# Kernel tuning notes

Hardware: AMD Instinct MI355X
Metric: run time of the kernel (lower is better)

The kernel has to match this reference:

```python
import jax, jax.numpy as jnp
import numpy as np

N = 1024
H = 128


def setup_inputs() -> dict:
    key = jax.random.key(0)
    k1, k2, k3, k4, k5, k6 = jax.random.split(key, 6)
    s = 1.0 / np.sqrt(H)
    return {
        "node_feats": jax.random.normal(k1, (N, H), dtype=jnp.float32),
        "edge_attr": jax.random.normal(k2, (N * N, H), dtype=jnp.float32),
        "We": jax.random.uniform(k3, (H, H), jnp.float32, -s, s),
        "be": jax.random.uniform(k4, (H,), jnp.float32, -s, s),
        "Wi": jax.random.uniform(k5, (H, H), jnp.float32, -s, s),
        "Wj": jax.random.uniform(k6, (H, H), jnp.float32, -s, s),
    }


def reference(node_feats, edge_attr, We, be, Wi, Wj):
    # f_ij: [N^2, H] linear with bias
    f_ij = edge_attr @ We.T + be
    # f_i, f_j: [N, H] linears without bias
    f_i = node_feats @ Wi.T
    f_j = node_feats @ Wj.T
    # torch.matmul on 1-D vectors -> scalar dot; broadcast into each H-wide row.
    dots = jnp.einsum("ih,jh->ij", f_i, f_j)  # [N, N]
    fi_fj = dots.reshape(-1, 1)                 # [N^2, 1], broadcasts over H
    return jax.nn.relu(f_ij + fi_fj)
```

## Files before the change

kernel.cpp:

```cpp
#include <hip/hip_runtime.h>
#include <hip/hip_bf16.h>
#include <stdint.h>
#include <stddef.h>

typedef __bf16 bf16_t;
typedef __bf16 bf16x8 __attribute__((ext_vector_type(8)));
typedef float  f32x4  __attribute__((ext_vector_type(4)));
typedef float  f32x16 __attribute__((ext_vector_type(16)));

#define NN 1024
#define H  128
#define GRID 2048

__global__ void k_proj(const float* __restrict__ node,
                       const float* __restrict__ Wi,
                       const float* __restrict__ Wj,
                       const float* __restrict__ We,
                       bf16_t* __restrict__ fi,
                       bf16_t* __restrict__ fj,
                       bf16_t* __restrict__ web) {
    __shared__ float nrow[H];
    const int row = blockIdx.x;
    const int t   = threadIdx.x;
    const int h   = t & (H - 1);
    const int sel = t >> 7;

    if (blockIdx.x < 64) {
        const int i = blockIdx.x * 256 + t;
        web[i] = (bf16_t)We[i];
    }

    if (t < H) nrow[t] = node[(size_t)row * H + t];
    __syncthreads();
    const float* w = (sel ? Wj : Wi) + (size_t)h * H;
    float acc = 0.f;
    #pragma unroll
    for (int k4 = 0; k4 < H / 4; ++k4) {
        f32x4 wv = *(const f32x4*)(w + k4 * 4);
        f32x4 nv = *(const f32x4*)(&nrow[k4 * 4]);
        acc += nv[0] * wv[0] + nv[1] * wv[1] + nv[2] * wv[2] + nv[3] * wv[3];
    }
    bf16_t* dst = sel ? fj : fi;
    dst[(size_t)row * H + h] = (bf16_t)acc;
}

__global__ __launch_bounds__(256, 4)
void k_dots(const bf16_t* __restrict__ fi,
            const bf16_t* __restrict__ fj,
            float* __restrict__ dots) {
    const int t    = threadIdx.x;
    const int wave = t >> 6;
    const int lane = t & 63;
    const int l15  = lane & 15;
    const int g    = lane >> 4;

    const int bm    = blockIdx.x >> 3;
    const int bn    = blockIdx.x & 7;
    const int ibase = bm * 64 + wave * 16;
    const int jbase = bn * 128;

    f32x4 acc[8];
    #pragma unroll
    for (int nt = 0; nt < 8; ++nt) acc[nt] = (f32x4){0.f, 0.f, 0.f, 0.f};

    const bf16_t* a = fi + (size_t)(ibase + l15) * H + g * 8;

    #pragma unroll
    for (int kst = 0; kst < 4; ++kst) {
        bf16x8 af = *(const bf16x8*)(a + kst * 32);
        #pragma unroll
        for (int nt = 0; nt < 8; ++nt) {
            bf16x8 bf = *(const bf16x8*)(fj + (size_t)(jbase + nt * 16 + l15) * H + kst * 32 + g * 8);
            acc[nt] = __builtin_amdgcn_mfma_f32_16x16x32_bf16(af, bf, acc[nt], 0, 0, 0);
        }
    }

    const int rbase = ibase + g * 4;
    #pragma unroll
    for (int r = 0; r < 4; ++r)
        #pragma unroll
        for (int nt = 0; nt < 8; ++nt)
            dots[(size_t)(rbase + r) * NN + jbase + nt * 16 + l15] = acc[nt][r];
}

__global__ __launch_bounds__(256)
void k_main(const float* __restrict__ edge,
            const bf16_t* __restrict__ web,
            const float* __restrict__ be,
            const float* __restrict__ dots,
            float* __restrict__ out) {
    __shared__ __align__(16) float bufA[64][H];
    __shared__ __align__(16) float bufB[64][H];
    __shared__ float ldots[512];

    const int t    = threadIdx.x;
    const int w    = t >> 6;
    const int lane = t & 63;
    const int l31  = lane & 31;
    const int h    = lane >> 5;
    const int wm   = w & 1;
    const int wn   = w >> 1;
    const size_t base = (size_t)blockIdx.x * 512;

    ldots[t]       = dots[base + t];
    ldots[256 + t] = dots[base + 256 + t];

    bf16x8 wfr[2][8];
    {
        const bf16_t* wp = web + (size_t)(wn * 64 + l31) * H + h * 8;
        #pragma unroll
        for (int nt = 0; nt < 2; ++nt)
            #pragma unroll
            for (int kk = 0; kk < 8; ++kk)
                wfr[nt][kk] = *(const bf16x8*)(wp + (size_t)(nt * 32) * H + kk * 16);
    }
    float bias[2];
    #pragma unroll
    for (int nt = 0; nt < 2; ++nt) bias[nt] = be[wn * 64 + nt * 32 + l31];

    #define LOADT(K, V)                                                          \
        {                                                                        \
            const char* tb = (const char*)(edge + (base + (size_t)(K) * 64) * H); \
            _Pragma("unroll")                                                    \
            for (int i = 0; i < 8; ++i) {                                        \
                const int rr = w * 16 + 2 * i + h;                               \
                V[i] = *(const f32x4*)(tb + rr * 512 + ((l31 * 16) ^ ((rr & 7) << 4))); \
            }                                                                    \
        }
    #define WRITET(BUFP, V)                                                      \
        {                                                                        \
            _Pragma("unroll")                                                    \
            for (int i = 0; i < 8; ++i)                                          \
                *(f32x4*)((char*)&BUFP[w * 16 + 2 * i][0] + h * 512 + l31 * 16) = V[i]; \
        }

    #define LDS_BARRIER()                                                        \
        {                                                                        \
            __builtin_amdgcn_sched_barrier(0);                                   \
            asm volatile("s_waitcnt lgkmcnt(0)" ::: "memory");                   \
            __builtin_amdgcn_s_barrier();                                        \
            __builtin_amdgcn_sched_barrier(0);                                   \
        }

    {
        f32x4 v0[8];
        LOADT(0, v0)
        WRITET(bufA, v0)
    }

    const int sw = (l31 & 7) << 4;

    #pragma unroll 1
    for (int k = 0; k < 8; ++k) {
        LDS_BARRIER()

        f32x4 vn[8];
        if (k < 7) LOADT(k + 1, vn)

        const char* crow = (const char*)((k & 1) ? &bufB[0][0] : &bufA[0][0])
                         + (wm * 32 + l31) * 512;
        f32x4 ua[8], ub[8];
        #pragma unroll
        for (int kk = 0; kk < 8; ++kk) {
            ua[kk] = *(const f32x4*)(crow + ((kk * 64 + h * 32 +  0) ^ sw));
            ub[kk] = *(const f32x4*)(crow + ((kk * 64 + h * 32 + 16) ^ sw));
        }

        f32x4 dv[4];
        #pragma unroll
        for (int b = 0; b < 4; ++b)
            dv[b] = *(const f32x4*)(&ldots[k * 64 + wm * 32 + 4 * h + 8 * b]);

        f32x16 acc[2];
        #pragma unroll
        for (int nt = 0; nt < 2; ++nt)
            #pragma unroll
            for (int r = 0; r < 16; ++r)
                acc[nt][r] = bias[nt] + dv[r >> 2][r & 3];

        #pragma unroll
        for (int kk = 0; kk < 8; ++kk) {
            bf16x8 af;
            #pragma unroll
            for (int e = 0; e < 4; ++e) {
                af[e]     = (bf16_t)ua[kk][e];
                af[e + 4] = (bf16_t)ub[kk][e];
            }
            #pragma unroll
            for (int nt = 0; nt < 2; ++nt)
                acc[nt] = __builtin_amdgcn_mfma_f32_32x32x16_bf16(af, wfr[nt][kk], acc[nt], 0, 0, 0);
        }

        float* orow = out + (base + (size_t)k * 64 + wm * 32 + 4 * h) * H + wn * 64 + l31;
        #pragma unroll
        for (int nt = 0; nt < 2; ++nt)
            #pragma unroll
            for (int r = 0; r < 16; ++r)
                __builtin_nontemporal_store(
                    fmaxf(acc[nt][r], 0.f),
                    &orow[((r & 3) + 8 * (r >> 2)) * H + nt * 32]);

        if (k < 7) {
            if (k & 1) { WRITET(bufA, vn) }
            else       { WRITET(bufB, vn) }
        }
    }
    #undef LOADT
    #undef WRITET
    #undef LDS_BARRIER
}

extern "C" void kernel_launch(void* const* d_in, const int* in_sizes, int n_in,
                              void* d_out, int out_size, void* d_ws, size_t ws_size,
                              hipStream_t stream) {
    const float* node = (const float*)d_in[0];
    const float* edge = (const float*)d_in[1];
    const float* We   = (const float*)d_in[2];
    const float* be   = (const float*)d_in[3];
    const float* Wi   = (const float*)d_in[4];
    const float* Wj   = (const float*)d_in[5];
    float* out = (float*)d_out;

    char* w = (char*)d_ws;
    bf16_t* fi_bf = (bf16_t*)w;
    bf16_t* fj_bf = (bf16_t*)(w + (256 << 10));
    float*  dots  = (float*)(w + (512 << 10));
    bf16_t* web   = (bf16_t*)(w + (512 << 10) + (4 << 20));

    k_proj<<<NN, 256, 0, stream>>>(node, Wi, Wj, We, fi_bf, fj_bf, web);
    k_dots<<<128, 256, 0, stream>>>(fi_bf, fj_bf, dots);
    k_main<<<GRID, 256, 0, stream>>>(edge, web, be, dots, out);
}
```

Before: 235.3 us.

## Fuse node dot products into main kernel and widen LDS swizzle

Removes the separate MFMA dots kernel and its 4MB dots buffer. Each main-kernel block now computes its 512 fi·fj dot products in fp32 from fi/fj rows. The LDS XOR swizzle for edge tiles widens from 3 to 5 bits. This saves a launch and the dots write/read traffic, but adds per-block scalar FMA work and repeated reads of the 512KB fj array (likely served from L2) before the main pipeline starts.

```diff
diff --git a/kernel.cpp b/kernel.cpp
--- a/kernel.cpp
+++ b/kernel.cpp
@@ -16,8 +16,8 @@
                        const float* __restrict__ Wi,
                        const float* __restrict__ Wj,
                        const float* __restrict__ We,
-                       bf16_t* __restrict__ fi,
-                       bf16_t* __restrict__ fj,
+                       float* __restrict__ fi,
+                       float* __restrict__ fj,
                        bf16_t* __restrict__ web) {
     __shared__ float nrow[H];
     const int row = blockIdx.x;
@@ -40,58 +40,21 @@
         f32x4 nv = *(const f32x4*)(&nrow[k4 * 4]);
         acc += nv[0] * wv[0] + nv[1] * wv[1] + nv[2] * wv[2] + nv[3] * wv[3];
     }
-    bf16_t* dst = sel ? fj : fi;
-    dst[(size_t)row * H + h] = (bf16_t)acc;
-}
-
-__global__ __launch_bounds__(256, 4)
-void k_dots(const bf16_t* __restrict__ fi,
-            const bf16_t* __restrict__ fj,
-            float* __restrict__ dots) {
-    const int t    = threadIdx.x;
-    const int wave = t >> 6;
-    const int lane = t & 63;
-    const int l15  = lane & 15;
-    const int g    = lane >> 4;
-
-    const int bm    = blockIdx.x >> 3;
-    const int bn    = blockIdx.x & 7;
-    const int ibase = bm * 64 + wave * 16;
-    const int jbase = bn * 128;
-
-    f32x4 acc[8];
-    #pragma unroll
-    for (int nt = 0; nt < 8; ++nt) acc[nt] = (f32x4){0.f, 0.f, 0.f, 0.f};
-
-    const bf16_t* a = fi + (size_t)(ibase + l15) * H + g * 8;
-
-    #pragma unroll
-    for (int kst = 0; kst < 4; ++kst) {
-        bf16x8 af = *(const bf16x8*)(a + kst * 32);
-        #pragma unroll
-        for (int nt = 0; nt < 8; ++nt) {
-            bf16x8 bf = *(const bf16x8*)(fj + (size_t)(jbase + nt * 16 + l15) * H + kst * 32 + g * 8);
-            acc[nt] = __builtin_amdgcn_mfma_f32_16x16x32_bf16(af, bf, acc[nt], 0, 0, 0);
-        }
-    }
-
-    const int rbase = ibase + g * 4;
-    #pragma unroll
-    for (int r = 0; r < 4; ++r)
-        #pragma unroll
-        for (int nt = 0; nt < 8; ++nt)
-            dots[(size_t)(rbase + r) * NN + jbase + nt * 16 + l15] = acc[nt][r];
+    float* dst = sel ? fj : fi;
+    dst[(size_t)row * H + h] = acc;
 }
 
 __global__ __launch_bounds__(256)
 void k_main(const float* __restrict__ edge,
             const bf16_t* __restrict__ web,
             const float* __restrict__ be,
-            const float* __restrict__ dots,
+            const float* __restrict__ fi,
+            const float* __restrict__ fj,
             float* __restrict__ out) {
     __shared__ __align__(16) float bufA[64][H];
     __shared__ __align__(16) float bufB[64][H];
     __shared__ float ldots[512];
+    __shared__ __align__(16) float fish[H];
 
     const int t    = threadIdx.x;
     const int w    = t >> 6;
@@ -102,8 +65,25 @@
     const int wn   = w >> 1;
     const size_t base = (size_t)blockIdx.x * 512;
 
-    ldots[t]       = dots[base + t];
-    ldots[256 + t] = dots[base + 256 + t];
+    const int ii = blockIdx.x >> 1;
+    const int jb = (blockIdx.x & 1) << 9;
+    if (t < 32) ((f32x4*)fish)[t] = ((const f32x4*)(fi + (size_t)ii * H))[t];
+    __syncthreads();
+    {
+        const float* r0 = fj + (size_t)(jb + t) * H;
+        const float* r1 = fj + (size_t)(jb + 256 + t) * H;
+        float d0 = 0.f, d1 = 0.f;
+        #pragma unroll
+        for (int c = 0; c < 32; ++c) {
+            f32x4 a0 = ((const f32x4*)r0)[c];
+            f32x4 a1 = ((const f32x4*)r1)[c];
+            f32x4 fv = ((const f32x4*)fish)[c];
+            d0 += a0[0]*fv[0] + a0[1]*fv[1] + a0[2]*fv[2] + a0[3]*fv[3];
+            d1 += a1[0]*fv[0] + a1[1]*fv[1] + a1[2]*fv[2] + a1[3]*fv[3];
+        }
+        ldots[t]       = d0;
+        ldots[256 + t] = d1;
+    }
 
     bf16x8 wfr[2][8];
     {
@@ -124,7 +104,7 @@
             _Pragma("unroll")                                                    \
             for (int i = 0; i < 8; ++i) {                                        \
                 const int rr = w * 16 + 2 * i + h;                               \
-                V[i] = *(const f32x4*)(tb + rr * 512 + ((l31 * 16) ^ ((rr & 7) << 4))); \
+                V[i] = *(const f32x4*)(tb + rr * 512 + ((l31 * 16) ^ ((rr & 31) << 4))); \
             }                                                                    \
         }
     #define WRITET(BUFP, V)                                                      \
@@ -148,7 +128,7 @@
         WRITET(bufA, v0)
     }
 
-    const int sw = (l31 & 7) << 4;
+    const int sw = l31 << 4;
 
     #pragma unroll 1
     for (int k = 0; k < 8; ++k) {
@@ -222,12 +202,10 @@
     float* out = (float*)d_out;
 
     char* w = (char*)d_ws;
-    bf16_t* fi_bf = (bf16_t*)w;
-    bf16_t* fj_bf = (bf16_t*)(w + (256 << 10));
-    float*  dots  = (float*)(w + (512 << 10));
-    bf16_t* web   = (bf16_t*)(w + (512 << 10) + (4 << 20));
-
-    k_proj<<<NN, 256, 0, stream>>>(node, Wi, Wj, We, fi_bf, fj_bf, web);
-    k_dots<<<128, 256, 0, stream>>>(fi_bf, fj_bf, dots);
-    k_main<<<GRID, 256, 0, stream>>>(edge, web, be, dots, out);
+    float*  fi_f  = (float*)w;
+    float*  fj_f  = (float*)(w + (512 << 10));
+    bf16_t* web   = (bf16_t*)(w + (1 << 20));
+
+    k_proj<<<NN, 256, 0, stream>>>(node, Wi, Wj, We, fi_f, fj_f, web);
+    k_main<<<GRID, 256, 0, stream>>>(edge, web, be, fi_f, fj_f, out);
 }
```

After: 251.1 us. +6.7%, slower.
